# Optimization experiments

Hardware: AMD Instinct MI355X
Metric: run time of the kernel (lower is better)

The kernel has to match this reference:

```python
import jax, jax.numpy as jnp
import numpy as np
from jax import lax

B, C, H, W = 32, 3, 128, 128
HP, WP = 7, 7          # feature map after 4 stride-2 valid 3x3 convs on 128
GH, GW = 32, 32        # glimpse shape
BN_EPS = 1e-5


def _conv(x, w, b, stride):
    y = lax.conv_general_dilated(x, w, (stride, stride), 'VALID',
                                 dimension_numbers=('NCHW', 'OIHW', 'NCHW'))
    return y + b[None, :, None, None]


def _bn(x, g, be):
    # training-mode BatchNorm2d: biased batch stats over (N,H,W)
    m = x.mean(axis=(0, 2, 3), keepdims=True)
    v = ((x - m) ** 2).mean(axis=(0, 2, 3), keepdims=True)
    return g[None, :, None, None] * (x - m) * lax.rsqrt(v + BN_EPS) + be[None, :, None, None]


def setup_inputs() -> dict:
    key = jax.random.key(0)
    ks = jax.random.split(key, 16)
    def w_init(k, shape):
        fan_in = shape[1] * shape[2] * shape[3]
        return (jax.random.normal(k, shape, jnp.float32) / np.sqrt(fan_in)).astype(jnp.float32)
    chans = [3, 64, 64, 64, 64]
    inp = {}
    inp['img'] = jax.random.normal(ks[0], (B, C, H, W), jnp.float32)
    inp['eps_scale'] = jax.random.normal(ks[1], (B, HP, WP, 2), jnp.float32)
    inp['eps_shift'] = jax.random.normal(ks[2], (B, HP, WP, 2), jnp.float32)
    for i in range(4):
        inp[f'w{i+1}'] = w_init(ks[3 + i], (chans[i + 1], chans[i], 3, 3))
        inp[f'b{i+1}'] = jnp.zeros((chans[i + 1],), jnp.float32)
        inp[f'g{i+1}'] = jnp.ones((chans[i + 1],), jnp.float32)
        inp[f'be{i+1}'] = jnp.zeros((chans[i + 1],), jnp.float32)
    inp['wp'] = w_init(ks[10], (64, 64, 1, 1)); inp['bp'] = jnp.zeros((64,), jnp.float32)
    inp['wz'] = w_init(ks[11], (11, 64, 1, 1)); inp['bz'] = jnp.zeros((11,), jnp.float32)
    return inp


def reference(img, eps_scale, eps_shift,
              w1, b1, g1, be1, w2, b2, g2, be2,
              w3, b3, g3, be3, w4, b4, g4, be4,
              wp, bp, wz, bz):
    h = img
    for (w, b, g, be) in ((w1, b1, g1, be1), (w2, b2, g2, be2),
                          (w3, b3, g3, be3), (w4, b4, g4, be4)):
        h = jax.nn.elu(_bn(_conv(h, w, b, 2), g, be))
    feats = jax.nn.elu(_conv(h, wp, bp, 1))            # [B,64,HP,WP]

    # --- znet and latent splits (only scale/shift affect returned glimpses) ---
    Z = _conv(feats, wz, bz, 1).transpose(0, 2, 3, 1)  # [B,HP,WP,11]
    smean, slogstd = Z[..., 3:5], Z[..., 5:7]
    shmean, shlogstd = Z[..., 7:9], Z[..., 9:11]
    z_scale = smean + jax.nn.softplus(slogstd) * eps_scale
    z_shift = shmean + jax.nn.softplus(shlogstd) * eps_shift

    glimpse_hw = jnp.array([GH, GW], jnp.float32)
    image_hw = jnp.array([H, W], jnp.float32)
    fmap_hw = jnp.array([HP, WP], jnp.float32)
    scale_img = jax.nn.sigmoid(z_scale) * glimpse_hw / image_hw   # [B,HP,WP,2] (h,w)
    shift_img = jax.nn.sigmoid(z_shift) / fmap_hw                 # [B,HP,WP,2] (i,j)

    ii = jnp.arange(HP, dtype=jnp.float32) / HP
    jj = jnp.arange(WP, dtype=jnp.float32) / WP
    ij = jnp.stack(jnp.meshgrid(ii, jj, indexing='ij'), axis=-1)  # [HP,WP,2]
    center = (ij[None] + shift_img) * 2.0 - 1.0                   # [B,HP,WP,2] in [-1,1]

    K = HP * WP
    th = scale_img[..., 0].reshape(B, K)   # height scale
    tw = scale_img[..., 1].reshape(B, K)   # width scale
    tx = center[..., 0].reshape(B, K)      # row (y) center
    ty = center[..., 1].reshape(B, K)      # col (x) center

    # affine_grid (align_corners=False) base coords; theta = [[tw,0,ty],[0,th,tx]]
    xb = (2.0 * jnp.arange(GW, dtype=jnp.float32) + 1.0) / GW - 1.0
    yb = (2.0 * jnp.arange(GH, dtype=jnp.float32) + 1.0) / GH - 1.0
    ixn = tw[:, :, None, None] * xb[None, None, None, :] + ty[:, :, None, None]  # [B,K,1,GW]
    iyn = th[:, :, None, None] * yb[None, None, :, None] + tx[:, :, None, None]  # [B,K,GH,1]
    # normalized -> pixel coords (align_corners=False)
    px = jnp.broadcast_to(((ixn + 1.0) * W - 1.0) * 0.5, (B, K, GH, GW))
    py = jnp.broadcast_to(((iyn + 1.0) * H - 1.0) * 0.5, (B, K, GH, GW))

    def sample_one(im, pxb, pyb):
        # im [C,H,W]; pxb/pyb [K,GH,GW]; bilinear, zero padding
        x0 = jnp.floor(pxb); y0 = jnp.floor(pyb)
        wx1 = pxb - x0; wy1 = pyb - y0
        x0i = x0.astype(jnp.int32); y0i = y0.astype(jnp.int32)
        x1i = x0i + 1; y1i = y0i + 1
        def g(yi, xi):
            m = ((xi >= 0) & (xi < W) & (yi >= 0) & (yi < H)).astype(im.dtype)
            v = im[:, jnp.clip(yi, 0, H - 1), jnp.clip(xi, 0, W - 1)]  # [C,K,GH,GW]
            return v * m[None]
        return (g(y0i, x0i) * ((1 - wy1) * (1 - wx1))[None]
                + g(y0i, x1i) * ((1 - wy1) * wx1)[None]
                + g(y1i, x0i) * (wy1 * (1 - wx1))[None]
                + g(y1i, x1i) * (wy1 * wx1)[None])

    xs = jax.vmap(sample_one)(img, px, py)            # [B,C,K,GH,GW]
    return xs.transpose(0, 2, 1, 3, 4).reshape(B * K, C, GH, GW)
```

## Files before the change

kernel.cpp:

```cpp
#include <hip/hip_runtime.h>
#include <math.h>

#define BATCH 32

__device__ __forceinline__ float eluf(float v) { return v > 0.f ? v : expm1f(v); }
__device__ __forceinline__ float softplusf(float x) {
    return fmaxf(x, 0.f) + log1pf(expf(-fabsf(x)));
}
__device__ __forceinline__ float sigmoidf(float x) { return 1.f / (1.f + expf(-x)); }

template <int CIN, int HIN, int WIN, int HOUT, int WOUT, int G, int BLOCK>
__global__ __launch_bounds__(BLOCK, 8) void conv_kernel(
    const float* __restrict__ in, const float* __restrict__ w, const float* __restrict__ bias,
    float* __restrict__ out, float* __restrict__ stats)
{
    constexpr int NW = BLOCK / 64;
    __shared__ float red_s[NW][G];
    __shared__ float red_q[NW][G];

    const int b   = blockIdx.x;
    const int co0 = blockIdx.y * G;
    const int t   = threadIdx.x;
    const int px  = blockIdx.z * BLOCK + t;
    const bool active = px < HOUT * WOUT;
    const int p = active ? px : 0;
    const int y = p / WOUT, x = p % WOUT;

    const float* ib = in + (size_t)b * CIN * HIN * WIN + (2 * y) * WIN + 2 * x;

    float acc[G];
#pragma unroll
    for (int u = 0; u < G; ++u) acc[u] = bias[co0 + u];

#pragma unroll 2
    for (int ci = 0; ci < CIN; ++ci) {
        const float* ip = ib + (size_t)ci * (HIN * WIN);
        float pch[9];
#pragma unroll
        for (int ky = 0; ky < 3; ++ky)
#pragma unroll
            for (int kx = 0; kx < 3; ++kx)
                pch[ky * 3 + kx] = ip[ky * WIN + kx];

        const float* wc = w + ((size_t)co0 * CIN + ci) * 9;
#pragma unroll
        for (int u = 0; u < G; ++u)
#pragma unroll
            for (int j = 0; j < 9; ++j)
                acc[u] = fmaf(pch[j], wc[u * CIN * 9 + j], acc[u]);
    }

    const int lane = t & 63, wv_ = t >> 6;
#pragma unroll
    for (int u = 0; u < G; ++u) {
        float v = active ? acc[u] : 0.f;
        if (active)
            out[(((size_t)b * 64 + co0 + u) * HOUT + y) * WOUT + x] = v;
        float s = v, q = v * v;
#pragma unroll
        for (int off = 32; off > 0; off >>= 1) {
            s += __shfl_down(s, off);
            q += __shfl_down(q, off);
        }
        if (lane == 0) { red_s[wv_][u] = s; red_q[wv_][u] = q; }
    }
    __syncthreads();
    if (t < 2 * G) {
        const int u = t >> 1, which = t & 1;
        float tt = 0.f;
#pragma unroll
        for (int k = 0; k < NW; ++k) tt += which ? red_q[k][u] : red_s[k][u];
        atomicAdd(&stats[2 * (co0 + u) + which], tt);
    }
}

template <int PLANE>
__global__ __launch_bounds__(256) void bnelu_kernel(
    float* __restrict__ h, const float* __restrict__ stats,
    const float* __restrict__ g, const float* __restrict__ be)
{
    const float invN = 1.f / (float)(BATCH * PLANE);
    const long long total = (long long)BATCH * 64 * PLANE;
    for (long long idx = (long long)blockIdx.x * blockDim.x + threadIdx.x; idx < total;
         idx += (long long)gridDim.x * blockDim.x) {
        int c = (int)((idx / PLANE) & 63);
        float s = stats[2 * c], q = stats[2 * c + 1];
        float m = s * invN;
        float var = fmaf(q, invN, -m * m);
        float a = g[c] * rsqrtf(var + 1e-5f);
        float bb = fmaf(-a, m, be[c]);
        h[idx] = eluf(fmaf(a, h[idx], bb));
    }
}

__global__ __launch_bounds__(256) void head_kernel(
    const float* __restrict__ x4, const float* __restrict__ stats4,
    const float* __restrict__ g4, const float* __restrict__ be4,
    const float* __restrict__ wp, const float* __restrict__ bp,
    const float* __restrict__ wz, const float* __restrict__ bz,
    const float* __restrict__ eps_scale, const float* __restrict__ eps_shift,
    float* __restrict__ params)
{
    __shared__ float xs[64 * 49];
    __shared__ float fe[64 * 49];
    __shared__ float zz[11 * 49];
    __shared__ float ha[64], hb[64];
    const int b = blockIdx.x, t = threadIdx.x;

    if (t < 64) {
        constexpr float invN = 1.f / (float)(BATCH * 49);
        float s = stats4[2 * t], q = stats4[2 * t + 1];
        float m = s * invN;
        float var = fmaf(q, invN, -m * m);
        float a = g4[t] * rsqrtf(var + 1e-5f);
        ha[t] = a;
        hb[t] = fmaf(-a, m, be4[t]);
    }
    __syncthreads();

    for (int i = t; i < 64 * 49; i += 256) {
        int c = i / 49;
        xs[i] = eluf(fmaf(ha[c], x4[(size_t)b * 64 * 49 + i], hb[c]));
    }
    __syncthreads();

    for (int i = t; i < 64 * 49; i += 256) {
        int co = i / 49, p = i % 49;
        float a = bp[co];
        for (int ci = 0; ci < 64; ++ci) a = fmaf(xs[ci * 49 + p], wp[co * 64 + ci], a);
        fe[i] = eluf(a);
    }
    __syncthreads();

    for (int i = t; i < 11 * 49; i += 256) {
        int co = i / 49, p = i % 49;
        float a = bz[co];
        for (int ci = 0; ci < 64; ++ci) a = fmaf(fe[ci * 49 + p], wz[co * 64 + ci], a);
        zz[i] = a;
    }
    __syncthreads();

    if (t < 49) {
        const int i = t / 7, j = t % 7;
        float es0 = eps_scale[((size_t)b * 49 + t) * 2 + 0];
        float es1 = eps_scale[((size_t)b * 49 + t) * 2 + 1];
        float eh0 = eps_shift[((size_t)b * 49 + t) * 2 + 0];
        float eh1 = eps_shift[((size_t)b * 49 + t) * 2 + 1];
        float zs0 = zz[3 * 49 + t] + softplusf(zz[5 * 49 + t]) * es0;
        float zs1 = zz[4 * 49 + t] + softplusf(zz[6 * 49 + t]) * es1;
        float zh0 = zz[7 * 49 + t] + softplusf(zz[9 * 49 + t]) * eh0;
        float zh1 = zz[8 * 49 + t] + softplusf(zz[10 * 49 + t]) * eh1;
        float th = sigmoidf(zs0) * 0.25f;
        float tw = sigmoidf(zs1) * 0.25f;
        float tx = ((float)i / 7.0f + sigmoidf(zh0) / 7.0f) * 2.f - 1.f;
        float ty = ((float)j / 7.0f + sigmoidf(zh1) / 7.0f) * 2.f - 1.f;
        float4* pp = (float4*)params;
        pp[b * 49 + t] = make_float4(th, tw, tx, ty);
    }
}

__device__ __forceinline__ float tap(const float* __restrict__ im, int yy, int xx) {
    bool ok = (xx >= 0) & (xx < 128) & (yy >= 0) & (yy < 128);
    int yc = min(max(yy, 0), 127);
    int xc = min(max(xx, 0), 127);
    return ok ? im[yc * 128 + xc] : 0.f;
}

__global__ __launch_bounds__(256) void sampler_kernel(
    const float* __restrict__ img, const float* __restrict__ params,
    float* __restrict__ out)
{
    const int bk = blockIdx.x;
    const int b  = bk / 49;
    const float4 pr = ((const float4*)params)[bk];
    const float th = pr.x, tw = pr.y, tx = pr.z, ty = pr.w;

    for (int idx = threadIdx.x; idx < 3072; idx += 256) {
        const int c  = idx >> 10;
        const int gy = (idx >> 5) & 31;
        const int gx = idx & 31;
        float xb = (2.f * gx + 1.f) / 32.f - 1.f;
        float yb = (2.f * gy + 1.f) / 32.f - 1.f;
        float ixn = fmaf(tw, xb, ty);
        float iyn = fmaf(th, yb, tx);
        float px = ((ixn + 1.f) * 128.f - 1.f) * 0.5f;
        float py = ((iyn + 1.f) * 128.f - 1.f) * 0.5f;
        float x0f = floorf(px), y0f = floorf(py);
        float wx = px - x0f, wy = py - y0f;
        int x0 = (int)x0f, y0 = (int)y0f;
        const float* im = img + ((size_t)b * 3 + c) * 16384;
        float v00 = tap(im, y0, x0);
        float v01 = tap(im, y0, x0 + 1);
        float v10 = tap(im, y0 + 1, x0);
        float v11 = tap(im, y0 + 1, x0 + 1);
        float r = v00 * (1.f - wy) * (1.f - wx) + v01 * (1.f - wy) * wx +
                  v10 * wy * (1.f - wx)        + v11 * wy * wx;
        out[(size_t)bk * 3072 + idx] = r;
    }
}

extern "C" void kernel_launch(void* const* d_in, const int* in_sizes, int n_in,
                              void* d_out, int out_size, void* d_ws, size_t ws_size,
                              hipStream_t stream)
{
    const float* img       = (const float*)d_in[0];
    const float* eps_scale = (const float*)d_in[1];
    const float* eps_shift = (const float*)d_in[2];
    const float* w1 = (const float*)d_in[3],  *b1 = (const float*)d_in[4];
    const float* g1 = (const float*)d_in[5],  *be1 = (const float*)d_in[6];
    const float* w2 = (const float*)d_in[7],  *b2 = (const float*)d_in[8];
    const float* g2 = (const float*)d_in[9],  *be2 = (const float*)d_in[10];
    const float* w3 = (const float*)d_in[11], *b3 = (const float*)d_in[12];
    const float* g3 = (const float*)d_in[13], *be3 = (const float*)d_in[14];
    const float* w4 = (const float*)d_in[15], *b4 = (const float*)d_in[16];
    const float* g4 = (const float*)d_in[17], *be4 = (const float*)d_in[18];
    const float* wp = (const float*)d_in[19], *bp = (const float*)d_in[20];
    const float* wz = (const float*)d_in[21], *bz = (const float*)d_in[22];

    float* ws     = (float*)d_ws;
    float* stats  = ws;
    float* params = ws + 512;
    float* h1     = ws + 6784;
    float* h2     = h1 + (size_t)32 * 64 * 63 * 63;
    float* h3     = h2 + (size_t)32 * 64 * 31 * 31;
    float* h4     = h3 + (size_t)32 * 64 * 15 * 15;

    float* outp = (float*)d_out;

    hipMemsetAsync(stats, 0, 512 * sizeof(float), stream);

    conv_kernel<3, 128, 128, 63, 63, 8, 256>
        <<<dim3(32, 8, 16), 256, 0, stream>>>(img, w1, b1, h1, stats + 0);
    bnelu_kernel<63 * 63><<<2048, 256, 0, stream>>>(h1, stats + 0, g1, be1);

    conv_kernel<64, 63, 63, 31, 31, 4, 256>
        <<<dim3(32, 16, 4), 256, 0, stream>>>(h1, w2, b2, h2, stats + 128);
    bnelu_kernel<31 * 31><<<2048, 256, 0, stream>>>(h2, stats + 128, g2, be2);

    conv_kernel<64, 31, 31, 15, 15, 2, 256>
        <<<dim3(32, 32, 1), 256, 0, stream>>>(h2, w3, b3, h3, stats + 256);
    bnelu_kernel<15 * 15><<<1024, 256, 0, stream>>>(h3, stats + 256, g3, be3);

    conv_kernel<64, 15, 15, 7, 7, 1, 64>
        <<<dim3(32, 64, 1), 64, 0, stream>>>(h3, w4, b4, h4, stats + 384);

    head_kernel<<<32, 256, 0, stream>>>(h4, stats + 384, g4, be4, wp, bp, wz, bz,
                                        eps_scale, eps_shift, params);

    sampler_kernel<<<1568, 256, 0, stream>>>(img, params, outp);
}
```

Before: 205.0 us.

## Pad activation rows to even strides, vectorize patch loads, replace stat atomics with partials

```diff
diff --git a/kernel.cpp b/kernel.cpp
--- a/kernel.cpp
+++ b/kernel.cpp
@@ -9,10 +9,11 @@
 }
 __device__ __forceinline__ float sigmoidf(float x) { return 1.f / (1.f + expf(-x)); }
 
-template <int CIN, int HIN, int WIN, int HOUT, int WOUT, int G, int BLOCK>
-__global__ __launch_bounds__(BLOCK, 8) void conv_kernel(
+template <int CIN, int HIN, int WIN, int RSIN, int HOUT, int WOUT, int RSOUT,
+          int G, int BLOCK, int NZ>
+__global__ __launch_bounds__(BLOCK, 6) void conv_kernel(
     const float* __restrict__ in, const float* __restrict__ w, const float* __restrict__ bias,
-    float* __restrict__ out, float* __restrict__ stats)
+    float* __restrict__ out, float* __restrict__ ps, float* __restrict__ pq)
 {
     constexpr int NW = BLOCK / 64;
     __shared__ float red_s[NW][G];
@@ -26,7 +27,7 @@
     const int p = active ? px : 0;
     const int y = p / WOUT, x = p % WOUT;
 
-    const float* ib = in + (size_t)b * CIN * HIN * WIN + (2 * y) * WIN + 2 * x;
+    const float* ib = in + (size_t)b * CIN * HIN * RSIN + (2 * y) * RSIN + 2 * x;
 
     float acc[G];
 #pragma unroll
@@ -34,13 +35,14 @@
 
 #pragma unroll 2
     for (int ci = 0; ci < CIN; ++ci) {
-        const float* ip = ib + (size_t)ci * (HIN * WIN);
-        float pch[9];
-#pragma unroll
-        for (int ky = 0; ky < 3; ++ky)
-#pragma unroll
-            for (int kx = 0; kx < 3; ++kx)
-                pch[ky * 3 + kx] = ip[ky * WIN + kx];
+        const float* ip = ib + (size_t)ci * (HIN * RSIN);
+        float2 a0 = *(const float2*)(ip);
+        float2 a1 = *(const float2*)(ip + RSIN);
+        float2 a2 = *(const float2*)(ip + 2 * RSIN);
+        float  c0 = ip[2];
+        float  c1 = ip[RSIN + 2];
+        float  c2 = ip[2 * RSIN + 2];
+        const float pch[9] = {a0.x, a0.y, c0, a1.x, a1.y, c1, a2.x, a2.y, c2};
 
         const float* wc = w + ((size_t)co0 * CIN + ci) * 9;
 #pragma unroll
@@ -50,40 +52,60 @@
                 acc[u] = fmaf(pch[j], wc[u * CIN * 9 + j], acc[u]);
     }
 
-    const int lane = t & 63, wv_ = t >> 6;
+    const int lane = t & 63, wv = t >> 6;
 #pragma unroll
     for (int u = 0; u < G; ++u) {
         float v = active ? acc[u] : 0.f;
         if (active)
-            out[(((size_t)b * 64 + co0 + u) * HOUT + y) * WOUT + x] = v;
+            out[((size_t)(b * 64 + co0 + u) * HOUT + y) * RSOUT + x] = v;
         float s = v, q = v * v;
 #pragma unroll
         for (int off = 32; off > 0; off >>= 1) {
             s += __shfl_down(s, off);
             q += __shfl_down(q, off);
         }
-        if (lane == 0) { red_s[wv_][u] = s; red_q[wv_][u] = q; }
+        if (lane == 0) { red_s[wv][u] = s; red_q[wv][u] = q; }
     }
     __syncthreads();
     if (t < 2 * G) {
-        const int u = t >> 1, which = t & 1;
+        const int u = t & (G - 1);
+        const bool wantq = t >= G;
         float tt = 0.f;
 #pragma unroll
-        for (int k = 0; k < NW; ++k) tt += which ? red_q[k][u] : red_s[k][u];
-        atomicAdd(&stats[2 * (co0 + u) + which], tt);
-    }
-}
-
-template <int PLANE>
+        for (int k = 0; k < NW; ++k) tt += wantq ? red_q[k][u] : red_s[k][u];
+        const int slot = (b * NZ + blockIdx.z) * 64 + co0 + u;
+        (wantq ? pq : ps)[slot] = tt;
+    }
+}
+
+template <int P>
+__global__ __launch_bounds__(128) void finalize_kernel(
+    const float* __restrict__ ps, const float* __restrict__ pq, float* __restrict__ stats)
+{
+    __shared__ float ls[128], lq[128];
+    const int c = blockIdx.x, t = threadIdx.x;
+    float s = 0.f, q = 0.f;
+    for (int pp = t; pp < P; pp += 128) { s += ps[pp * 64 + c]; q += pq[pp * 64 + c]; }
+    ls[t] = s; lq[t] = q;
+    __syncthreads();
+#pragma unroll
+    for (int off = 64; off > 0; off >>= 1) {
+        if (t < off) { ls[t] += ls[t + off]; lq[t] += lq[t + off]; }
+        __syncthreads();
+    }
+    if (t == 0) { stats[2 * c] = ls[0]; stats[2 * c + 1] = lq[0]; }
+}
+
+template <int PLANE_PAD, int NREAL>
 __global__ __launch_bounds__(256) void bnelu_kernel(
     float* __restrict__ h, const float* __restrict__ stats,
     const float* __restrict__ g, const float* __restrict__ be)
 {
-    const float invN = 1.f / (float)(BATCH * PLANE);
-    const long long total = (long long)BATCH * 64 * PLANE;
+    const float invN = 1.f / (float)(BATCH * NREAL);
+    const long long total = (long long)BATCH * 64 * PLANE_PAD;
     for (long long idx = (long long)blockIdx.x * blockDim.x + threadIdx.x; idx < total;
          idx += (long long)gridDim.x * blockDim.x) {
-        int c = (int)((idx / PLANE) & 63);
+        int c = (int)((idx / PLANE_PAD) & 63);
         float s = stats[2 * c], q = stats[2 * c + 1];
         float m = s * invN;
         float var = fmaf(q, invN, -m * m);
@@ -119,8 +141,9 @@
     __syncthreads();
 
     for (int i = t; i < 64 * 49; i += 256) {
-        int c = i / 49;
-        xs[i] = eluf(fmaf(ha[c], x4[(size_t)b * 64 * 49 + i], hb[c]));
+        int c = i / 49, p = i % 49;
+        float v = x4[(size_t)b * 64 * 56 + c * 56 + (p / 7) * 8 + (p % 7)];
+        xs[i] = eluf(fmaf(ha[c], v, hb[c]));
     }
     __syncthreads();
 
@@ -220,29 +243,33 @@
     float* ws     = (float*)d_ws;
     float* stats  = ws;
     float* params = ws + 512;
-    float* h1     = ws + 6784;
-    float* h2     = h1 + (size_t)32 * 64 * 63 * 63;
-    float* h3     = h2 + (size_t)32 * 64 * 31 * 31;
-    float* h4     = h3 + (size_t)32 * 64 * 15 * 15;
+    float* ps     = ws + 6784;
+    float* pq     = ws + 39552;
+    float* h1     = ws + 72320;
+    float* h2     = h1 + (size_t)32 * 64 * 63 * 64;
+    float* h3     = h2 + (size_t)32 * 64 * 31 * 32;
+    float* h4     = h3 + (size_t)32 * 64 * 15 * 16;
 
     float* outp = (float*)d_out;
 
-    hipMemsetAsync(stats, 0, 512 * sizeof(float), stream);
-
-    conv_kernel<3, 128, 128, 63, 63, 8, 256>
-        <<<dim3(32, 8, 16), 256, 0, stream>>>(img, w1, b1, h1, stats + 0);
-    bnelu_kernel<63 * 63><<<2048, 256, 0, stream>>>(h1, stats + 0, g1, be1);
-
-    conv_kernel<64, 63, 63, 31, 31, 4, 256>
-        <<<dim3(32, 16, 4), 256, 0, stream>>>(h1, w2, b2, h2, stats + 128);
-    bnelu_kernel<31 * 31><<<2048, 256, 0, stream>>>(h2, stats + 128, g2, be2);
-
-    conv_kernel<64, 31, 31, 15, 15, 2, 256>
-        <<<dim3(32, 32, 1), 256, 0, stream>>>(h2, w3, b3, h3, stats + 256);
-    bnelu_kernel<15 * 15><<<1024, 256, 0, stream>>>(h3, stats + 256, g3, be3);
-
-    conv_kernel<64, 15, 15, 7, 7, 1, 64>
-        <<<dim3(32, 64, 1), 64, 0, stream>>>(h3, w4, b4, h4, stats + 384);
+    conv_kernel<3, 128, 128, 128, 63, 63, 64, 8, 256, 16>
+        <<<dim3(32, 8, 16), 256, 0, stream>>>(img, w1, b1, h1, ps, pq);
+    finalize_kernel<512><<<64, 128, 0, stream>>>(ps, pq, stats + 0);
+    bnelu_kernel<63 * 64, 63 * 63><<<2048, 256, 0, stream>>>(h1, stats + 0, g1, be1);
+
+    conv_kernel<64, 63, 63, 64, 31, 31, 32, 8, 256, 4>
+        <<<dim3(32, 8, 4), 256, 0, stream>>>(h1, w2, b2, h2, ps, pq);
+    finalize_kernel<128><<<64, 128, 0, stream>>>(ps, pq, stats + 128);
+    bnelu_kernel<31 * 32, 31 * 31><<<2048, 256, 0, stream>>>(h2, stats + 128, g2, be2);
+
+    conv_kernel<64, 31, 31, 32, 15, 15, 16, 8, 256, 1>
+        <<<dim3(32, 8, 1), 256, 0, stream>>>(h2, w3, b3, h3, ps, pq);
+    finalize_kernel<32><<<64, 128, 0, stream>>>(ps, pq, stats + 256);
+    bnelu_kernel<15 * 16, 15 * 15><<<1024, 256, 0, stream>>>(h3, stats + 256, g3, be3);
+
+    conv_kernel<64, 15, 15, 16, 7, 7, 8, 8, 64, 1>
+        <<<dim3(32, 8, 1), 64, 0, stream>>>(h3, w4, b4, h4, ps, pq);
+    finalize_kernel<32><<<64, 128, 0, stream>>>(ps, pq, stats + 384);
 
     head_kernel<<<32, 256, 0, stream>>>(h4, stats + 384, g4, be4, wp, bp, wz, bz,
                                         eps_scale, eps_shift, params);
```

Measured after the change: 243.7 us. 1.19x slower.
